# Performance work log

Measured on AMD Instinct MI355X. Metric: run time of the kernel, lower is better.

Reference implementation:

```python
import jax, jax.numpy as jnp
import numpy as np

N_NODES = 32768
N_EDGES = 524288
IN_F = 256
OUT_F = 128
NB = 4


def setup_inputs() -> dict:
    key = jax.random.key(0)
    ks = jax.random.split(key, 12)
    s_in = 1.0 / np.sqrt(IN_F)
    s_out = 1.0 / np.sqrt(OUT_F)
    s_cat = 1.0 / np.sqrt(OUT_F * NB)
    return {
        "x": jax.random.normal(ks[0], (N_NODES, IN_F), dtype=jnp.float32),
        "edge_index": jax.random.randint(ks[1], (2, N_EDGES), 0, N_NODES, dtype=jnp.int64),
        "Wb": jax.random.uniform(ks[2], (NB, IN_F, OUT_F), jnp.float32, -s_in, s_in),
        "bb": jax.random.uniform(ks[3], (NB, OUT_F), jnp.float32, -s_in, s_in),
        "W1": jax.random.uniform(ks[4], (NB, OUT_F, OUT_F), jnp.float32, -s_out, s_out),
        "b1": jax.random.uniform(ks[5], (NB, OUT_F), jnp.float32, -s_out, s_out),
        "W2": jax.random.uniform(ks[6], (NB, OUT_F, OUT_F), jnp.float32, -s_out, s_out),
        "b2": jax.random.uniform(ks[7], (NB, OUT_F), jnp.float32, -s_out, s_out),
        "branch_gates": jnp.ones((NB,), dtype=jnp.float32),
        "temperature": jnp.asarray(1.0, dtype=jnp.float32),
        "Wo": jax.random.uniform(ks[8], (OUT_F * NB, OUT_F), jnp.float32, -s_cat, s_cat),
        "bo": jax.random.uniform(ks[9], (OUT_F,), jnp.float32, -s_cat, s_cat),
    }


def _scatter_mean_step(h, row, col, inv_deg):
    # gather per-edge source features, mean-reduce onto destination nodes
    sums = jax.ops.segment_sum(h[row], col, num_segments=N_NODES)
    return sums * inv_deg


def reference(x, edge_index, Wb, bb, W1, b1, W2, b2, branch_gates, temperature, Wo, bo):
    row, col = edge_index[0], edge_index[1]
    deg = jax.ops.segment_sum(jnp.ones((N_EDGES,), x.dtype), col, num_segments=N_NODES)
    inv_deg = (1.0 / jnp.maximum(deg, 1.0))[:, None]  # empty segments -> 0 (scatter_mean semantics)

    gates = jax.nn.softmax(branch_gates / temperature)

    branch_outputs = []
    for i in range(NB):
        h = x @ Wb[i] + bb[i]                   # [N, OUT_F]
        for _ in range(i):                       # scale = scales[i % 4] = i
            h = _scatter_mean_step(h, row, col, inv_deg)
        h = jax.nn.relu(h @ W1[i] + b1[i]) @ W2[i] + b2[i]
        branch_outputs.append(h * gates[i])

    concat = jnp.concatenate(branch_outputs, axis=1)  # [N, NB*OUT_F]
    return concat @ Wo + bo
```

## Files before the change

### kernel.cpp

```cpp
#include <hip/hip_runtime.h>
#include <math.h>

#define N_NODES 32768
#define N_EDGES 524288
#define IN_F    256
#define OUT_F   128
#define NB      4

typedef __attribute__((ext_vector_type(8))) short bf16x8;
typedef __attribute__((ext_vector_type(4))) float f32x4;

__device__ __forceinline__ ushort f2b(float f) {
    uint u = __float_as_uint(f);
    return (ushort)((u + 0x7fffu + ((u >> 16) & 1u)) >> 16);
}
__device__ __forceinline__ float b2f_lo(uint v) { return __uint_as_float(v << 16); }
__device__ __forceinline__ float b2f_hi(uint v) { return __uint_as_float(v & 0xffff0000u); }

__device__ __forceinline__ float softmax_gate(const float* bg, const float* temp, int i) {
    float T = temp[0];
    float mx = fmaxf(fmaxf(bg[0], bg[1]), fmaxf(bg[2], bg[3]));
    float e0 = expf((bg[0] - mx) / T), e1 = expf((bg[1] - mx) / T);
    float e2 = expf((bg[2] - mx) / T), e3 = expf((bg[3] - mx) / T);
    float s = e0 + e1 + e2 + e3;
    float ei = (i == 0) ? e0 : (i == 1) ? e1 : (i == 2) ? e2 : e3;
    return ei / s;
}

__global__ void detect_kernel(const int* __restrict__ ei, int* __restrict__ flag) {
    int t = threadIdx.x;
    if (ei[2 * t + 1] != 0) atomicOr(flag, 1);
}

__global__ __launch_bounds__(256) void count_conv_kernel(
    const int* __restrict__ ei, const int* __restrict__ flag, int* __restrict__ deg,
    const float* __restrict__ x, ushort* __restrict__ xb) {
    int b = blockIdx.x;
    if (b < N_EDGES / 256) {
        int e = b * 256 + threadIdx.x;
        int c = (*flag == 0) ? ei[2 * (N_EDGES + e)] : ei[N_EDGES + e];
        atomicAdd(&deg[c], 1);
    } else {
        int idx = (b - N_EDGES / 256) * 256 + threadIdx.x;
        float4 v = ((const float4*)x)[idx];
        ushort4 o;
        o.x = f2b(v.x); o.y = f2b(v.y); o.z = f2b(v.z); o.w = f2b(v.w);
        ((ushort4*)xb)[idx] = o;
    }
}

__global__ __launch_bounds__(256) void scan1_kernel(const int* __restrict__ deg,
                                                    int* __restrict__ bsum) {
    int t = threadIdx.x;
    int v = deg[blockIdx.x * 256 + t];
    __shared__ int red[4];
    int lane = t & 63, wv = t >> 6;
#pragma unroll
    for (int off = 32; off > 0; off >>= 1) v += __shfl_down(v, off);
    if (lane == 0) red[wv] = v;
    __syncthreads();
    if (t == 0) bsum[blockIdx.x] = red[0] + red[1] + red[2] + red[3];
}

__global__ __launch_bounds__(128) void scan2_kernel(const int* __restrict__ bsum,
                                                    int* __restrict__ bbase,
                                                    int* __restrict__ offs) {
    __shared__ int s[128];
    int t = threadIdx.x;
    int v = bsum[t];
    s[t] = v;
    __syncthreads();
    for (int off = 1; off < 128; off <<= 1) {
        int add = (t >= off) ? s[t - off] : 0;
        __syncthreads();
        s[t] += add;
        __syncthreads();
    }
    bbase[t] = s[t] - v;
    if (t == 127) offs[N_NODES] = s[127];
}

__global__ __launch_bounds__(256) void scan3_kernel(
    const int* __restrict__ deg, const int* __restrict__ bbase,
    int* __restrict__ offs, int* __restrict__ cursor,
    float* __restrict__ invd, float* __restrict__ m1) {
    __shared__ int s[256];
    int t = threadIdx.x;
    int idx = blockIdx.x * 256 + t;
    int d = deg[idx];
    s[t] = d;
    __syncthreads();
    for (int off = 1; off < 256; off <<= 1) {
        int add = (t >= off) ? s[t - off] : 0;
        __syncthreads();
        s[t] += add;
        __syncthreads();
    }
    int excl = bbase[blockIdx.x] + s[t] - d;
    offs[idx] = excl;
    cursor[idx] = excl;
    invd[idx] = 1.0f / (float)((d > 1) ? d : 1);
    m1[idx] = (d > 0) ? 1.0f : 0.0f;
}

__global__ __launch_bounds__(256) void fill_prep_kernel(
    const int* __restrict__ ei, const int* __restrict__ flag,
    int* __restrict__ cursor, int* __restrict__ srcs,
    const float* __restrict__ Wb, const float* __restrict__ W1,
    const float* __restrict__ W2, const float* __restrict__ Wo,
    const float* __restrict__ bb, const float* __restrict__ b2,
    const float* __restrict__ bo, const float* __restrict__ bg,
    const float* __restrict__ temp,
    ushort* __restrict__ WcT, ushort* __restrict__ WzT,
    float* __restrict__ u, float* __restrict__ cvec) {
    __shared__ float smem[16 * 128];
    int b = blockIdx.x;
    int tid = threadIdx.x;
    if (b < N_EDGES / 256) {
        int e = b * 256 + tid;
        int r, c;
        if (*flag == 0) { r = ei[2 * e]; c = ei[2 * (N_EDGES + e)]; }
        else            { r = ei[e];     c = ei[N_EDGES + e]; }
        int slot = atomicAdd(&cursor[c], 1);
        srcs[slot] = r;
        return;
    }
    int f = tid & 127, rh = tid >> 7;
    if (b < N_EDGES / 256 + 64) {
        int id = b - N_EDGES / 256;
        int i = id >> 4, k0 = (id & 15) * 16;
#pragma unroll
        for (int rr = 0; rr < 8; rr++)
            smem[(rh * 8 + rr) * 128 + f] = Wb[((size_t)i * IN_F + k0 + rh * 8 + rr) * OUT_F + f];
        __syncthreads();
        float acc[8] = {};
        const float* W1i = W1 + (size_t)i * OUT_F * OUT_F;
        for (int j = 0; j < OUT_F; j++) {
            float w1 = W1i[j * OUT_F + f];
#pragma unroll
            for (int rr = 0; rr < 8; rr++) acc[rr] += smem[(rh * 8 + rr) * 128 + j] * w1;
        }
        ushort tmp[8];
#pragma unroll
        for (int rr = 0; rr < 8; rr++) tmp[rr] = f2b(acc[rr]);
        *(uint4*)(WcT + ((size_t)i * OUT_F + f) * IN_F + k0 + rh * 8) = *(uint4*)tmp;
    } else if (b < N_EDGES / 256 + 96) {
        int id = b - (N_EDGES / 256 + 64);
        int i = id >> 3, j0 = (id & 7) * 16;
#pragma unroll
        for (int rr = 0; rr < 8; rr++)
            smem[(rh * 8 + rr) * 128 + f] = W2[((size_t)i * OUT_F + j0 + rh * 8 + rr) * OUT_F + f];
        __syncthreads();
        float acc[8] = {};
        for (int l = 0; l < OUT_F; l++) {
            float wo = Wo[((size_t)i * OUT_F + l) * OUT_F + f];
#pragma unroll
            for (int rr = 0; rr < 8; rr++) acc[rr] += smem[(rh * 8 + rr) * 128 + l] * wo;
        }
        float g = softmax_gate(bg, temp, i);
        ushort tmp[8];
#pragma unroll
        for (int rr = 0; rr < 8; rr++) tmp[rr] = f2b(g * acc[rr]);
        *(uint4*)(WzT + (size_t)f * (NB * OUT_F) + i * OUT_F + j0 + rh * 8) = *(uint4*)tmp;
    } else {
        int id = b - (N_EDGES / 256 + 96);
        int jc = rh;
        if (id < NB) {
            int i = id;
            float partial = 0.f;
            for (int j = jc * 64; j < jc * 64 + 64; j++)
                partial += bb[i * OUT_F + j] * W1[((size_t)i * OUT_F + j) * OUT_F + f];
            smem[jc * 128 + f] = partial;
            __syncthreads();
            if (jc == 0) u[i * OUT_F + f] = smem[f] + smem[128 + f];
        } else {
            int i = id - NB;
            float partial = 0.f;
            for (int j = jc * 64; j < jc * 64 + 64; j++)
                partial += b2[i * OUT_F + j] * Wo[((size_t)i * OUT_F + j) * OUT_F + f];
            smem[jc * 128 + f] = partial;
            __syncthreads();
            if (jc == 0) {
                float tot = (smem[f] + smem[128 + f]) * softmax_gate(bg, temp, i);
                if (i == 0) tot += bo[f];
                atomicAdd(&cvec[f], tot);
            }
        }
    }
}

#define GATHER_256(INBUF)                                                       \
    float a0[8] = {0.f,0.f,0.f,0.f,0.f,0.f,0.f,0.f};                            \
    float a1[8] = {0.f,0.f,0.f,0.f,0.f,0.f,0.f,0.f};                            \
    int p = s;                                                                  \
    for (; p + 8 <= e; p += 8) {                                                \
        int base = p + 4 * half;                                                \
        int2 s01 = *(const int2*)(srcs + base);                                 \
        int2 s23 = *(const int2*)(srcs + base + 2);                             \
        uint4 v0 = *(const uint4*)(INBUF + (size_t)s01.x * IN_F + fl * 8);      \
        uint4 v1 = *(const uint4*)(INBUF + (size_t)s01.y * IN_F + fl * 8);      \
        uint4 v2 = *(const uint4*)(INBUF + (size_t)s23.x * IN_F + fl * 8);      \
        uint4 v3 = *(const uint4*)(INBUF + (size_t)s23.y * IN_F + fl * 8);      \
        ACC8(a0, v0); ACC8(a1, v1); ACC8(a0, v2); ACC8(a1, v3);                 \
    }                                                                           \
    for (; p + 4 <= e; p += 4) {                                                \
        int2 ss = *(const int2*)(srcs + p + 2 * half);                          \
        uint4 v0 = *(const uint4*)(INBUF + (size_t)ss.x * IN_F + fl * 8);       \
        uint4 v1 = *(const uint4*)(INBUF + (size_t)ss.y * IN_F + fl * 8);       \
        ACC8(a0, v0); ACC8(a1, v1);                                             \
    }                                                                           \
    for (; p + half < e; p += 2) {                                              \
        int src = srcs[p + half];                                               \
        uint4 v0 = *(const uint4*)(INBUF + (size_t)src * IN_F + fl * 8);        \
        ACC8(a0, v0);                                                           \
    }                                                                           \
    _Pragma("unroll") for (int k = 0; k < 8; k++) a0[k] += a1[k];               \
    _Pragma("unroll") for (int k = 0; k < 8; k++) a0[k] += __shfl_down(a0[k], 32);

#define ACC8(A, V)                                                              \
    A[0] += b2f_lo(V.x); A[1] += b2f_hi(V.x);                                   \
    A[2] += b2f_lo(V.y); A[3] += b2f_hi(V.y);                                   \
    A[4] += b2f_lo(V.z); A[5] += b2f_hi(V.z);                                   \
    A[6] += b2f_lo(V.w); A[7] += b2f_hi(V.w)

__global__ __launch_bounds__(256) void prop_x_kernel(
    const ushort* __restrict__ in, ushort* __restrict__ out,
    const float* __restrict__ m_in, float* __restrict__ m_out,
    const int* __restrict__ offs, const int* __restrict__ srcs,
    const float* __restrict__ invd) {
    int blk = blockIdx.x;
    if (blk >= N_NODES / 4) {
        int n = (blk - N_NODES / 4) * 256 + threadIdx.x;
        int s = offs[n], e = offs[n + 1];
        float sum = 0.f;
        for (int p = s; p < e; ++p) sum += m_in[srcs[p]];
        m_out[n] = sum * invd[n];
        return;
    }
    int node = blk * 4 + (threadIdx.x >> 6);
    int lane = threadIdx.x & 63;
    int half = lane >> 5, fl = lane & 31;
    int s = offs[node], e = offs[node + 1];
    GATHER_256(in);
    if (half == 0) {
        float w = invd[node];
        uint4 o;
        o.x = (uint)f2b(a0[0] * w) | ((uint)f2b(a0[1] * w) << 16);
        o.y = (uint)f2b(a0[2] * w) | ((uint)f2b(a0[3] * w) << 16);
        o.z = (uint)f2b(a0[4] * w) | ((uint)f2b(a0[5] * w) << 16);
        o.w = (uint)f2b(a0[6] * w) | ((uint)f2b(a0[7] * w) << 16);
        *(uint4*)(out + (size_t)node * IN_F + fl * 8) = o;
    }
}

__global__ __launch_bounds__(256) void prop_pq_kernel(
    const ushort* __restrict__ PQ, ushort* __restrict__ R, ushort* __restrict__ Qp,
    const float* __restrict__ m2, float* __restrict__ m3,
    const float* __restrict__ u2, const float* __restrict__ b12,
    const int* __restrict__ offs, const int* __restrict__ srcs,
    const float* __restrict__ invd) {
    int blk = blockIdx.x;
    if (blk >= N_NODES / 4) {
        int n = (blk - N_NODES / 4) * 256 + threadIdx.x;
        int s = offs[n], e = offs[n + 1];
        float sum = 0.f;
        for (int p = s; p < e; ++p) sum += m2[srcs[p]];
        m3[n] = sum * invd[n];
        return;
    }
    int node = blk * 4 + (threadIdx.x >> 6);
    int lane = threadIdx.x & 63;
    int half = lane >> 5, fl = lane & 31;
    int s = offs[node], e = offs[node + 1];
    GATHER_256(PQ);
    if (half == 0) {
        float w = invd[node];
        if (fl < 16) {
            int col = fl * 8;
            float mv = m2[node];
            float4 ua = *(const float4*)(u2 + col);
            float4 ub = *(const float4*)(u2 + col + 4);
            float4 ba = *(const float4*)(b12 + col);
            float4 bb_ = *(const float4*)(b12 + col + 4);
            float o_[8];
            o_[0] = fmaxf(a0[0] * w + mv * ua.x + ba.x, 0.f);
            o_[1] = fmaxf(a0[1] * w + mv * ua.y + ba.y, 0.f);
            o_[2] = fmaxf(a0[2] * w + mv * ua.z + ba.z, 0.f);
            o_[3] = fmaxf(a0[3] * w + mv * ua.w + ba.w, 0.f);
            o_[4] = fmaxf(a0[4] * w + mv * ub.x + bb_.x, 0.f);
            o_[5] = fmaxf(a0[5] * w + mv * ub.y + bb_.y, 0.f);
            o_[6] = fmaxf(a0[6] * w + mv * ub.z + bb_.z, 0.f);
            o_[7] = fmaxf(a0[7] * w + mv * ub.w + bb_.w, 0.f);
            uint4 o;
            o.x = (uint)f2b(o_[0]) | ((uint)f2b(o_[1]) << 16);
            o.y = (uint)f2b(o_[2]) | ((uint)f2b(o_[3]) << 16);
            o.z = (uint)f2b(o_[4]) | ((uint)f2b(o_[5]) << 16);
            o.w = (uint)f2b(o_[6]) | ((uint)f2b(o_[7]) << 16);
            *(uint4*)(R + (size_t)node * (NB * OUT_F) + 2 * OUT_F + col) = o;
        } else {
            int col = (fl - 16) * 8;
            uint4 o;
            o.x = (uint)f2b(a0[0] * w) | ((uint)f2b(a0[1] * w) << 16);
            o.y = (uint)f2b(a0[2] * w) | ((uint)f2b(a0[3] * w) << 16);
            o.z = (uint)f2b(a0[4] * w) | ((uint)f2b(a0[5] * w) << 16);
            o.w = (uint)f2b(a0[6] * w) | ((uint)f2b(a0[7] * w) << 16);
            *(uint4*)(Qp + (size_t)node * OUT_F + col) = o;
        }
    }
}

__global__ __launch_bounds__(256) void prop_q_kernel(
    const ushort* __restrict__ Qp, ushort* __restrict__ R,
    const float* __restrict__ m3, const float* __restrict__ u3,
    const float* __restrict__ b13,
    const int* __restrict__ offs, const int* __restrict__ srcs,
    const float* __restrict__ invd) {
    int node = blockIdx.x * 4 + (threadIdx.x >> 6);
    int lane = threadIdx.x & 63;
    int q = lane >> 4, fl = lane & 15;
    int s = offs[node], e = offs[node + 1];
    float a[8] = {0.f,0.f,0.f,0.f,0.f,0.f,0.f,0.f};
    float b[8] = {0.f,0.f,0.f,0.f,0.f,0.f,0.f,0.f};
    int p = s;
    for (; p + 8 <= e; p += 8) {
        int2 ss = *(const int2*)(srcs + p + 2 * q);
        uint4 v0 = *(const uint4*)(Qp + (size_t)ss.x * OUT_F + fl * 8);
        uint4 v1 = *(const uint4*)(Qp + (size_t)ss.y * OUT_F + fl * 8);
        ACC8(a, v0); ACC8(b, v1);
    }
    for (; p + 4 <= e; p += 4) {
        int src = srcs[p + q];
        uint4 v0 = *(const uint4*)(Qp + (size_t)src * OUT_F + fl * 8);
        ACC8(a, v0);
    }
    if (p + q < e) {
        int src = srcs[p + q];
        uint4 v0 = *(const uint4*)(Qp + (size_t)src * OUT_F + fl * 8);
        ACC8(a, v0);
    }
#pragma unroll
    for (int k = 0; k < 8; k++) a[k] += b[k];
#pragma unroll
    for (int k = 0; k < 8; k++) a[k] += __shfl_down(a[k], 32);
#pragma unroll
    for (int k = 0; k < 8; k++) a[k] += __shfl_down(a[k], 16);
    if (lane < 16) {
        float w = invd[node];
        float mv = m3[node];
        int col = fl * 8;
        float4 ua = *(const float4*)(u3 + col);
        float4 ub = *(const float4*)(u3 + col + 4);
        float4 ba = *(const float4*)(b13 + col);
        float4 bb_ = *(const float4*)(b13 + col + 4);
        float o_[8];
        o_[0] = fmaxf(a[0] * w + mv * ua.x + ba.x, 0.f);
        o_[1] = fmaxf(a[1] * w + mv * ua.y + ba.y, 0.f);
        o_[2] = fmaxf(a[2] * w + mv * ua.z + ba.z, 0.f);
        o_[3] = fmaxf(a[3] * w + mv * ua.w + ba.w, 0.f);
        o_[4] = fmaxf(a[4] * w + mv * ub.x + bb_.x, 0.f);
        o_[5] = fmaxf(a[5] * w + mv * ub.y + bb_.y, 0.f);
        o_[6] = fmaxf(a[6] * w + mv * ub.z + bb_.z, 0.f);
        o_[7] = fmaxf(a[7] * w + mv * ub.w + bb_.w, 0.f);
        uint4 o;
        o.x = (uint)f2b(o_[0]) | ((uint)f2b(o_[1]) << 16);
        o.y = (uint)f2b(o_[2]) | ((uint)f2b(o_[3]) << 16);
        o.z = (uint)f2b(o_[4]) | ((uint)f2b(o_[5]) << 16);
        o.w = (uint)f2b(o_[6]) | ((uint)f2b(o_[7]) << 16);
        *(uint4*)(R + (size_t)node * (NB * OUT_F) + 3 * OUT_F + col) = o;
    }
}

__global__ __launch_bounds__(256) void gemmP_kernel(
    const ushort* __restrict__ xb, const ushort* __restrict__ X1b,
    const ushort* __restrict__ WcT, const float* __restrict__ u,
    const float* __restrict__ b1, const float* __restrict__ m1,
    ushort* __restrict__ R, ushort* __restrict__ PQ) {
    int y = blockIdx.y;
    const ushort* A = (y == 0) ? xb : X1b;
    const ushort* WT = WcT + (size_t)y * OUT_F * IN_F;
    int m0 = blockIdx.x * 128;

    __shared__ ushort As[128][72];
    __shared__ ushort Bs[128][72];

    int tid = threadIdx.x;
    int wv = tid >> 6, lane = tid & 63, quad = lane >> 4, lm = lane & 15;

    f32x4 acc[2][8];
    f32x4 zero = {0.f, 0.f, 0.f, 0.f};
#pragma unroll
    for (int i = 0; i < 2; i++)
#pragma unroll
        for (int j = 0; j < 8; j++) acc[i][j] = zero;

    for (int k0 = 0; k0 < IN_F; k0 += 64) {
        __syncthreads();
#pragma unroll
        for (int it = 0; it < 4; it++) {
            int c = tid + 256 * it;
            int r = c >> 3, c8 = c & 7;
            *(uint4*)&As[r][c8 * 8] = *(const uint4*)(A + (size_t)(m0 + r) * IN_F + k0 + c8 * 8);
            *(uint4*)&Bs[r][c8 * 8] = *(const uint4*)(WT + (size_t)r * IN_F + k0 + c8 * 8);
        }
        __syncthreads();
#pragma unroll
        for (int ks = 0; ks < 2; ks++) {
            bf16x8 af0 = *(const bf16x8*)&As[wv * 32 + lm][ks * 32 + quad * 8];
            bf16x8 af1 = *(const bf16x8*)&As[wv * 32 + 16 + lm][ks * 32 + quad * 8];
#pragma unroll
            for (int nt = 0; nt < 8; nt++) {
                bf16x8 bf = *(const bf16x8*)&Bs[nt * 16 + lm][ks * 32 + quad * 8];
                acc[0][nt] = __builtin_amdgcn_mfma_f32_16x16x32_bf16(af0, bf, acc[0][nt], 0, 0, 0);
                acc[1][nt] = __builtin_amdgcn_mfma_f32_16x16x32_bf16(af1, bf, acc[1][nt], 0, 0, 0);
            }
        }
    }

    if (y >= 2) {
        int pqoff = (y - 2) * OUT_F;
#pragma unroll
        for (int mt = 0; mt < 2; mt++)
#pragma unroll
            for (int r = 0; r < 4; r++) {
                int row = m0 + wv * 32 + mt * 16 + quad * 4 + r;
#pragma unroll
                for (int nt = 0; nt < 8; nt++) {
                    int col = nt * 16 + lm;
                    PQ[(size_t)row * IN_F + pqoff + col] = f2b(acc[mt][nt][r]);
                }
            }
    } else {
        float uv[8], bv[8];
#pragma unroll
        for (int nt = 0; nt < 8; nt++) {
            int col = nt * 16 + lm;
            uv[nt] = u[y * OUT_F + col];
            bv[nt] = b1[y * OUT_F + col];
        }
#pragma unroll
        for (int mt = 0; mt < 2; mt++)
#pragma unroll
            for (int r = 0; r < 4; r++) {
                int row = m0 + wv * 32 + mt * 16 + quad * 4 + r;
                float mval = (y == 0) ? 1.0f : m1[row];
#pragma unroll
                for (int nt = 0; nt < 8; nt++) {
                    int col = nt * 16 + lm;
                    float h = acc[mt][nt][r] + mval * uv[nt] + bv[nt];
                    R[(size_t)row * (NB * OUT_F) + y * OUT_F + col] = f2b(fmaxf(h, 0.f));
                }
            }
    }
}

__global__ __launch_bounds__(256) void gemm2_mfma_kernel(
    const ushort* __restrict__ R, const ushort* __restrict__ WzT,
    const float* __restrict__ cvec, float* __restrict__ out) {
    int m0 = blockIdx.x * 128;
    const int K = NB * OUT_F;

    __shared__ ushort As[128][72];
    __shared__ ushort Bs[128][72];

    int tid = threadIdx.x;
    int wv = tid >> 6, lane = tid & 63, quad = lane >> 4, lm = lane & 15;

    f32x4 acc[2][8];
    f32x4 zero = {0.f, 0.f, 0.f, 0.f};
#pragma unroll
    for (int i = 0; i < 2; i++)
#pragma unroll
        for (int j = 0; j < 8; j++) acc[i][j] = zero;

    for (int k0 = 0; k0 < K; k0 += 64) {
        __syncthreads();
#pragma unroll
        for (int it = 0; it < 4; it++) {
            int c = tid + 256 * it;
            int r = c >> 3, c8 = c & 7;
            *(uint4*)&As[r][c8 * 8] = *(const uint4*)(R + (size_t)(m0 + r) * K + k0 + c8 * 8);
            *(uint4*)&Bs[r][c8 * 8] = *(const uint4*)(WzT + (size_t)r * K + k0 + c8 * 8);
        }
        __syncthreads();
#pragma unroll
        for (int ks = 0; ks < 2; ks++) {
            bf16x8 af0 = *(const bf16x8*)&As[wv * 32 + lm][ks * 32 + quad * 8];
            bf16x8 af1 = *(const bf16x8*)&As[wv * 32 + 16 + lm][ks * 32 + quad * 8];
#pragma unroll
            for (int nt = 0; nt < 8; nt++) {
                bf16x8 bf = *(const bf16x8*)&Bs[nt * 16 + lm][ks * 32 + quad * 8];
                acc[0][nt] = __builtin_amdgcn_mfma_f32_16x16x32_bf16(af0, bf, acc[0][nt], 0, 0, 0);
                acc[1][nt] = __builtin_amdgcn_mfma_f32_16x16x32_bf16(af1, bf, acc[1][nt], 0, 0, 0);
            }
        }
    }

    float cb[8];
#pragma unroll
    for (int nt = 0; nt < 8; nt++) cb[nt] = cvec[nt * 16 + lm];
#pragma unroll
    for (int mt = 0; mt < 2; mt++)
#pragma unroll
        for (int r = 0; r < 4; r++) {
            int row = m0 + wv * 32 + mt * 16 + quad * 4 + r;
#pragma unroll
            for (int nt = 0; nt < 8; nt++) {
                int col = nt * 16 + lm;
                out[(size_t)row * OUT_F + col] = acc[mt][nt][r] + cb[nt];
            }
        }
}

extern "C" void kernel_launch(void* const* d_in, const int* in_sizes, int n_in,
                              void* d_out, int out_size, void* d_ws, size_t ws_size,
                              hipStream_t stream) {
    const float* x    = (const float*)d_in[0];
    const int*   ei   = (const int*)d_in[1];
    const float* Wb   = (const float*)d_in[2];
    const float* bb   = (const float*)d_in[3];
    const float* W1   = (const float*)d_in[4];
    const float* b1   = (const float*)d_in[5];
    const float* W2   = (const float*)d_in[6];
    const float* b2   = (const float*)d_in[7];
    const float* bg   = (const float*)d_in[8];
    const float* temp = (const float*)d_in[9];
    const float* Wo   = (const float*)d_in[10];
    const float* bo   = (const float*)d_in[11];
    float* out = (float*)d_out;

    char* w = (char*)d_ws;
    size_t used = 0;
    auto alloc = [&](size_t bytes) {
        char* p = w + used;
        used += (bytes + 255) & ~(size_t)255;
        return p;
    };
    int*    deg    = (int*)alloc(N_NODES * 4);
    float*  cvec   = (float*)alloc(OUT_F * 4);
    int*    flag   = (int*)alloc(4);
    int*    offs   = (int*)alloc((N_NODES + 2) * 4);
    int*    cursor = (int*)alloc(N_NODES * 4);
    int*    srcs   = (int*)alloc(N_EDGES * 4);
    int*    bsum   = (int*)alloc(128 * 4);
    int*    bbase  = (int*)alloc(128 * 4);
    float*  invd   = (float*)alloc(N_NODES * 4);
    float*  mbuf   = (float*)alloc((size_t)3 * N_NODES * 4);
    float*  u      = (float*)alloc(NB * OUT_F * 4);
    ushort* WcT    = (ushort*)alloc((size_t)NB * IN_F * OUT_F * 2);
    ushort* WzT    = (ushort*)alloc((size_t)NB * OUT_F * OUT_F * 2);
    ushort* xb     = (ushort*)alloc((size_t)N_NODES * IN_F * 2);
    ushort* X1b    = (ushort*)alloc((size_t)N_NODES * IN_F * 2);
    ushort* PQ     = (ushort*)alloc((size_t)N_NODES * IN_F * 2);
    ushort* Qp     = (ushort*)alloc((size_t)N_NODES * OUT_F * 2);
    ushort* R      = (ushort*)alloc((size_t)N_NODES * NB * OUT_F * 2);
    if (used > ws_size) return;

    float* m1v = mbuf;
    float* m2v = mbuf + N_NODES;
    float* m3v = mbuf + 2 * N_NODES;

    hipMemsetAsync(deg, 0, N_NODES * 4 + 512 + 256, stream);

    detect_kernel<<<1, 64, 0, stream>>>(ei, flag);
    count_conv_kernel<<<N_EDGES / 256 + N_NODES * IN_F / 1024, 256, 0, stream>>>(
        ei, flag, deg, x, xb);
    scan1_kernel<<<N_NODES / 256, 256, 0, stream>>>(deg, bsum);
    scan2_kernel<<<1, 128, 0, stream>>>(bsum, bbase, offs);
    scan3_kernel<<<N_NODES / 256, 256, 0, stream>>>(deg, bbase, offs, cursor, invd, m1v);
    fill_prep_kernel<<<N_EDGES / 256 + 64 + 32 + 8, 256, 0, stream>>>(
        ei, flag, cursor, srcs, Wb, W1, W2, Wo, bb, b2, bo, bg, temp, WcT, WzT, u, cvec);

    prop_x_kernel<<<N_NODES / 4 + N_NODES / 256, 256, 0, stream>>>(
        xb, X1b, m1v, m2v, offs, srcs, invd);
    {
        dim3 grid(N_NODES / 128, NB);
        gemmP_kernel<<<grid, 256, 0, stream>>>(xb, X1b, WcT, u, b1, m1v, R, PQ);
    }
    prop_pq_kernel<<<N_NODES / 4 + N_NODES / 256, 256, 0, stream>>>(
        PQ, R, Qp, m2v, m3v, u + 2 * OUT_F, b1 + 2 * OUT_F, offs, srcs, invd);
    prop_q_kernel<<<N_NODES / 4, 256, 0, stream>>>(
        Qp, R, m3v, u + 3 * OUT_F, b1 + 3 * OUT_F, offs, srcs, invd);

    gemm2_mfma_kernel<<<N_NODES / 128, 256, 0, stream>>>(R, WzT, cvec, out);
}
```

Baseline: 308.4 us.

## Fuse independent GEMM tiles into gather kernels and merge prep launches

Moves branch-0 and branch-1 GEMMs into the gather/propagation kernels as extra blocks so the compute-bound MFMA tiles can run alongside memory-bound gathers. Only the branch-2/3 GEMM stays as a separate launch. The int32/int64 detection is folded into each kernel via a ballot, removing the detect launch and flag buffer. Weight prep and bf16 conversion now share a launch with degree counting, and the CSR fill becomes its own kernel. The cost is larger, more heterogeneous grids, higher LDS and register use per block for the gather blocks, and block-scheduling imbalance.

```diff
diff --git a/kernel.cpp b/kernel.cpp
--- a/kernel.cpp
+++ b/kernel.cpp
@@ -6,6 +6,12 @@
 #define IN_F    256
 #define OUT_F   128
 #define NB      4
+
+#define NE_BLK   (N_EDGES / 256)
+#define CONV_BLK (N_NODES * IN_F / 1024)
+#define GX_BLK   (N_NODES / 4)
+#define GEMM_BLK (N_NODES / 128)
+#define M_BLK    (N_NODES / 256)
 
 typedef __attribute__((ext_vector_type(8))) short bf16x8;
 typedef __attribute__((ext_vector_type(4))) float f32x4;
@@ -27,85 +33,18 @@
     return ei / s;
 }
 
-__global__ void detect_kernel(const int* __restrict__ ei, int* __restrict__ flag) {
-    int t = threadIdx.x;
-    if (ei[2 * t + 1] != 0) atomicOr(flag, 1);
-}
-
-__global__ __launch_bounds__(256) void count_conv_kernel(
-    const int* __restrict__ ei, const int* __restrict__ flag, int* __restrict__ deg,
-    const float* __restrict__ x, ushort* __restrict__ xb) {
-    int b = blockIdx.x;
-    if (b < N_EDGES / 256) {
-        int e = b * 256 + threadIdx.x;
-        int c = (*flag == 0) ? ei[2 * (N_EDGES + e)] : ei[N_EDGES + e];
-        atomicAdd(&deg[c], 1);
-    } else {
-        int idx = (b - N_EDGES / 256) * 256 + threadIdx.x;
-        float4 v = ((const float4*)x)[idx];
-        ushort4 o;
-        o.x = f2b(v.x); o.y = f2b(v.y); o.z = f2b(v.z); o.w = f2b(v.w);
-        ((ushort4*)xb)[idx] = o;
-    }
-}
-
-__global__ __launch_bounds__(256) void scan1_kernel(const int* __restrict__ deg,
-                                                    int* __restrict__ bsum) {
-    int t = threadIdx.x;
-    int v = deg[blockIdx.x * 256 + t];
-    __shared__ int red[4];
-    int lane = t & 63, wv = t >> 6;
-#pragma unroll
-    for (int off = 32; off > 0; off >>= 1) v += __shfl_down(v, off);
-    if (lane == 0) red[wv] = v;
+__device__ __forceinline__ int detect_i32(const int* __restrict__ ei, int* sflag) {
+    if (threadIdx.x < 64) {
+        unsigned long long b = __ballot(ei[2 * threadIdx.x + 1] != 0);
+        if (threadIdx.x == 0) *sflag = (b != 0ull) ? 1 : 0;
+    }
     __syncthreads();
-    if (t == 0) bsum[blockIdx.x] = red[0] + red[1] + red[2] + red[3];
-}
-
-__global__ __launch_bounds__(128) void scan2_kernel(const int* __restrict__ bsum,
-                                                    int* __restrict__ bbase,
-                                                    int* __restrict__ offs) {
-    __shared__ int s[128];
-    int t = threadIdx.x;
-    int v = bsum[t];
-    s[t] = v;
-    __syncthreads();
-    for (int off = 1; off < 128; off <<= 1) {
-        int add = (t >= off) ? s[t - off] : 0;
-        __syncthreads();
-        s[t] += add;
-        __syncthreads();
-    }
-    bbase[t] = s[t] - v;
-    if (t == 127) offs[N_NODES] = s[127];
-}
-
-__global__ __launch_bounds__(256) void scan3_kernel(
-    const int* __restrict__ deg, const int* __restrict__ bbase,
-    int* __restrict__ offs, int* __restrict__ cursor,
-    float* __restrict__ invd, float* __restrict__ m1) {
-    __shared__ int s[256];
-    int t = threadIdx.x;
-    int idx = blockIdx.x * 256 + t;
-    int d = deg[idx];
-    s[t] = d;
-    __syncthreads();
-    for (int off = 1; off < 256; off <<= 1) {
-        int add = (t >= off) ? s[t - off] : 0;
-        __syncthreads();
-        s[t] += add;
-        __syncthreads();
-    }
-    int excl = bbase[blockIdx.x] + s[t] - d;
-    offs[idx] = excl;
-    cursor[idx] = excl;
-    invd[idx] = 1.0f / (float)((d > 1) ? d : 1);
-    m1[idx] = (d > 0) ? 1.0f : 0.0f;
-}
-
-__global__ __launch_bounds__(256) void fill_prep_kernel(
-    const int* __restrict__ ei, const int* __restrict__ flag,
-    int* __restrict__ cursor, int* __restrict__ srcs,
+    return *sflag;
+}
+
+__global__ __launch_bounds__(256) void count_prep_kernel(
+    const int* __restrict__ ei, int* __restrict__ deg,
+    const float* __restrict__ x, ushort* __restrict__ xb,
     const float* __restrict__ Wb, const float* __restrict__ W1,
     const float* __restrict__ W2, const float* __restrict__ Wo,
     const float* __restrict__ bb, const float* __restrict__ b2,
@@ -114,21 +53,29 @@
     ushort* __restrict__ WcT, ushort* __restrict__ WzT,
     float* __restrict__ u, float* __restrict__ cvec) {
     __shared__ float smem[16 * 128];
+    __shared__ int sflag;
     int b = blockIdx.x;
     int tid = threadIdx.x;
-    if (b < N_EDGES / 256) {
+    if (b < NE_BLK) {
+        int i32 = detect_i32(ei, &sflag);
         int e = b * 256 + tid;
-        int r, c;
-        if (*flag == 0) { r = ei[2 * e]; c = ei[2 * (N_EDGES + e)]; }
-        else            { r = ei[e];     c = ei[N_EDGES + e]; }
-        int slot = atomicAdd(&cursor[c], 1);
-        srcs[slot] = r;
+        int c = (i32 == 0) ? ei[2 * (N_EDGES + e)] : ei[N_EDGES + e];
+        atomicAdd(&deg[c], 1);
         return;
     }
+    b -= NE_BLK;
+    if (b < CONV_BLK) {
+        int idx = b * 256 + tid;
+        float4 v = ((const float4*)x)[idx];
+        ushort4 o;
+        o.x = f2b(v.x); o.y = f2b(v.y); o.z = f2b(v.z); o.w = f2b(v.w);
+        ((ushort4*)xb)[idx] = o;
+        return;
+    }
+    b -= CONV_BLK;
     int f = tid & 127, rh = tid >> 7;
-    if (b < N_EDGES / 256 + 64) {
-        int id = b - N_EDGES / 256;
-        int i = id >> 4, k0 = (id & 15) * 16;
+    if (b < 64) {
+        int i = b >> 4, k0 = (b & 15) * 16;
 #pragma unroll
         for (int rr = 0; rr < 8; rr++)
             smem[(rh * 8 + rr) * 128 + f] = Wb[((size_t)i * IN_F + k0 + rh * 8 + rr) * OUT_F + f];
@@ -144,8 +91,8 @@
 #pragma unroll
         for (int rr = 0; rr < 8; rr++) tmp[rr] = f2b(acc[rr]);
         *(uint4*)(WcT + ((size_t)i * OUT_F + f) * IN_F + k0 + rh * 8) = *(uint4*)tmp;
-    } else if (b < N_EDGES / 256 + 96) {
-        int id = b - (N_EDGES / 256 + 64);
+    } else if (b < 96) {
+        int id = b - 64;
         int i = id >> 3, j0 = (id & 7) * 16;
 #pragma unroll
         for (int rr = 0; rr < 8; rr++)
@@ -163,7 +110,7 @@
         for (int rr = 0; rr < 8; rr++) tmp[rr] = f2b(g * acc[rr]);
         *(uint4*)(WzT + (size_t)f * (NB * OUT_F) + i * OUT_F + j0 + rh * 8) = *(uint4*)tmp;
     } else {
-        int id = b - (N_EDGES / 256 + 96);
+        int id = b - 96;
         int jc = rh;
         if (id < NB) {
             int i = id;
@@ -188,6 +135,78 @@
         }
     }
 }
+
+__global__ __launch_bounds__(256) void scan1_kernel(const int* __restrict__ deg,
+                                                    int* __restrict__ bsum) {
+    int t = threadIdx.x;
+    int v = deg[blockIdx.x * 256 + t];
+    __shared__ int red[4];
+    int lane = t & 63, wv = t >> 6;
+#pragma unroll
+    for (int off = 32; off > 0; off >>= 1) v += __shfl_down(v, off);
+    if (lane == 0) red[wv] = v;
+    __syncthreads();
+    if (t == 0) bsum[blockIdx.x] = red[0] + red[1] + red[2] + red[3];
+}
+
+__global__ __launch_bounds__(128) void scan2_kernel(const int* __restrict__ bsum,
+                                                    int* __restrict__ bbase,
+                                                    int* __restrict__ offs) {
+    __shared__ int s[128];
+    int t = threadIdx.x;
+    int v = bsum[t];
+    s[t] = v;
+    __syncthreads();
+    for (int off = 1; off < 128; off <<= 1) {
+        int add = (t >= off) ? s[t - off] : 0;
+        __syncthreads();
+        s[t] += add;
+        __syncthreads();
+    }
+    bbase[t] = s[t] - v;
+    if (t == 127) offs[N_NODES] = s[127];
+}
+
+__global__ __launch_bounds__(256) void scan3_kernel(
+    const int* __restrict__ deg, const int* __restrict__ bbase,
+    int* __restrict__ offs, int* __restrict__ cursor,
+    float* __restrict__ invd, float* __restrict__ m1) {
+    __shared__ int s[256];
+    int t = threadIdx.x;
+    int idx = blockIdx.x * 256 + t;
+    int d = deg[idx];
+    s[t] = d;
+    __syncthreads();
+    for (int off = 1; off < 256; off <<= 1) {
+        int add = (t >= off) ? s[t - off] : 0;
+        __syncthreads();
+        s[t] += add;
+        __syncthreads();
+    }
+    int excl = bbase[blockIdx.x] + s[t] - d;
+    offs[idx] = excl;
+    cursor[idx] = excl;
+    invd[idx] = 1.0f / (float)((d > 1) ? d : 1);
+    m1[idx] = (d > 0) ? 1.0f : 0.0f;
+}
+
+__global__ __launch_bounds__(256) void fill_kernel(
+    const int* __restrict__ ei, int* __restrict__ cursor, int* __restrict__ srcs) {
+    __shared__ int sflag;
+    int i32 = detect_i32(ei, &sflag);
+    int e = blockIdx.x * 256 + threadIdx.x;
+    int r, c;
+    if (i32 == 0) { r = ei[2 * e]; c = ei[2 * (N_EDGES + e)]; }
+    else          { r = ei[e];     c = ei[N_EDGES + e]; }
+    int slot = atomicAdd(&cursor[c], 1);
+    srcs[slot] = r;
+}
+
+#define ACC8(A, V)                                                              \
+    A[0] += b2f_lo(V.x); A[1] += b2f_hi(V.x);                                   \
+    A[2] += b2f_lo(V.y); A[3] += b2f_hi(V.y);                                   \
+    A[4] += b2f_lo(V.z); A[5] += b2f_hi(V.z);                                   \
+    A[6] += b2f_lo(V.w); A[7] += b2f_hi(V.w)
 
 #define GATHER_256(INBUF)                                                       \
     float a0[8] = {0.f,0.f,0.f,0.f,0.f,0.f,0.f,0.f};                            \
@@ -217,31 +236,81 @@
     _Pragma("unroll") for (int k = 0; k < 8; k++) a0[k] += a1[k];               \
     _Pragma("unroll") for (int k = 0; k < 8; k++) a0[k] += __shfl_down(a0[k], 32);
 
-#define ACC8(A, V)                                                              \
-    A[0] += b2f_lo(V.x); A[1] += b2f_hi(V.x);                                   \
-    A[2] += b2f_lo(V.y); A[3] += b2f_hi(V.y);                                   \
-    A[4] += b2f_lo(V.z); A[5] += b2f_hi(V.z);                                   \
-    A[6] += b2f_lo(V.w); A[7] += b2f_hi(V.w)
-
-__global__ __launch_bounds__(256) void prop_x_kernel(
-    const ushort* __restrict__ in, ushort* __restrict__ out,
-    const float* __restrict__ m_in, float* __restrict__ m_out,
+#define GEMM_TILE_BODY(APTR, WTPTR, UPTR, BPTR, MEXPR, RCOL)                    \
+    int m0 = gblk * 128;                                                        \
+    int wv = tid >> 6, lane = tid & 63, quad = lane >> 4, lm = lane & 15;       \
+    f32x4 acc[2][8];                                                            \
+    f32x4 zero = {0.f, 0.f, 0.f, 0.f};                                          \
+    _Pragma("unroll") for (int i = 0; i < 2; i++)                               \
+        _Pragma("unroll") for (int j = 0; j < 8; j++) acc[i][j] = zero;         \
+    for (int k0 = 0; k0 < IN_F; k0 += 64) {                                     \
+        __syncthreads();                                                        \
+        _Pragma("unroll") for (int it = 0; it < 4; it++) {                      \
+            int c = tid + 256 * it;                                             \
+            int r = c >> 3, c8 = c & 7;                                         \
+            *(uint4*)&As[r][c8 * 8] =                                           \
+                *(const uint4*)(APTR + (size_t)(m0 + r) * IN_F + k0 + c8 * 8);  \
+            *(uint4*)&Bs[r][c8 * 8] =                                           \
+                *(const uint4*)(WTPTR + (size_t)r * IN_F + k0 + c8 * 8);        \
+        }                                                                       \
+        __syncthreads();                                                        \
+        _Pragma("unroll") for (int ks = 0; ks < 2; ks++) {                      \
+            bf16x8 af0 = *(const bf16x8*)&As[wv * 32 + lm][ks * 32 + quad * 8]; \
+            bf16x8 af1 = *(const bf16x8*)&As[wv * 32 + 16 + lm][ks * 32 + quad * 8]; \
+            _Pragma("unroll") for (int nt = 0; nt < 8; nt++) {                  \
+                bf16x8 bf = *(const bf16x8*)&Bs[nt * 16 + lm][ks * 32 + quad * 8]; \
+                acc[0][nt] = __builtin_amdgcn_mfma_f32_16x16x32_bf16(af0, bf, acc[0][nt], 0, 0, 0); \
+                acc[1][nt] = __builtin_amdgcn_mfma_f32_16x16x32_bf16(af1, bf, acc[1][nt], 0, 0, 0); \
+            }                                                                   \
+        }                                                                       \
+    }                                                                           \
+    float uv[8], bv[8];                                                         \
+    _Pragma("unroll") for (int nt = 0; nt < 8; nt++) {                          \
+        int col = nt * 16 + lm;                                                 \
+        uv[nt] = UPTR[col];                                                     \
+        bv[nt] = BPTR[col];                                                     \
+    }                                                                           \
+    _Pragma("unroll") for (int mt = 0; mt < 2; mt++)                            \
+        _Pragma("unroll") for (int r = 0; r < 4; r++) {                         \
+            int row = m0 + wv * 32 + mt * 16 + quad * 4 + r;                    \
+            float mval = (MEXPR);                                               \
+            _Pragma("unroll") for (int nt = 0; nt < 8; nt++) {                  \
+                int col = nt * 16 + lm;                                         \
+                float h = acc[mt][nt][r] + mval * uv[nt] + bv[nt];              \
+                R[(size_t)row * (NB * OUT_F) + (RCOL) + col] = f2b(fmaxf(h, 0.f)); \
+            }                                                                   \
+        }
+
+__global__ __launch_bounds__(256) void prop_x_gemm0_kernel(
+    const ushort* __restrict__ xb, ushort* __restrict__ X1b,
+    const float* __restrict__ m1, float* __restrict__ m2,
+    const ushort* __restrict__ WcT, const float* __restrict__ u,
+    const float* __restrict__ b1, ushort* __restrict__ R,
     const int* __restrict__ offs, const int* __restrict__ srcs,
     const float* __restrict__ invd) {
+    __shared__ ushort As[128][72];
+    __shared__ ushort Bs[128][72];
     int blk = blockIdx.x;
-    if (blk >= N_NODES / 4) {
-        int n = (blk - N_NODES / 4) * 256 + threadIdx.x;
+    int tid = threadIdx.x;
+    if (blk < GEMM_BLK) {
+        int gblk = blk;
+        GEMM_TILE_BODY(xb, WcT, u, b1, 1.0f, 0)
+        return;
+    }
+    blk -= GEMM_BLK;
+    if (blk >= GX_BLK) {
+        int n = (blk - GX_BLK) * 256 + tid;
         int s = offs[n], e = offs[n + 1];
         float sum = 0.f;
-        for (int p = s; p < e; ++p) sum += m_in[srcs[p]];
-        m_out[n] = sum * invd[n];
+        for (int p = s; p < e; ++p) sum += m1[srcs[p]];
+        m2[n] = sum * invd[n];
         return;
     }
-    int node = blk * 4 + (threadIdx.x >> 6);
-    int lane = threadIdx.x & 63;
+    int node = blk * 4 + (tid >> 6);
+    int lane = tid & 63;
     int half = lane >> 5, fl = lane & 31;
     int s = offs[node], e = offs[node + 1];
-    GATHER_256(in);
+    GATHER_256(xb);
     if (half == 0) {
         float w = invd[node];
         uint4 o;
@@ -249,27 +318,94 @@
         o.y = (uint)f2b(a0[2] * w) | ((uint)f2b(a0[3] * w) << 16);
         o.z = (uint)f2b(a0[4] * w) | ((uint)f2b(a0[5] * w) << 16);
         o.w = (uint)f2b(a0[6] * w) | ((uint)f2b(a0[7] * w) << 16);
-        *(uint4*)(out + (size_t)node * IN_F + fl * 8) = o;
-    }
-}
-
-__global__ __launch_bounds__(256) void prop_pq_kernel(
-    const ushort* __restrict__ PQ, ushort* __restrict__ R, ushort* __restrict__ Qp,
-    const float* __restrict__ m2, float* __restrict__ m3,
-    const float* __restrict__ u2, const float* __restrict__ b12,
+        *(uint4*)(X1b + (size_t)node * IN_F + fl * 8) = o;
+    }
+}
+
+__global__ __launch_bounds__(256) void gemmP23_kernel(
+    const ushort* __restrict__ X1b, const ushort* __restrict__ WcT,
+    ushort* __restrict__ PQ) {
+    int y = blockIdx.y + 2;
+    const ushort* WT = WcT + (size_t)y * OUT_F * IN_F;
+    int m0 = blockIdx.x * 128;
+    __shared__ ushort As[128][72];
+    __shared__ ushort Bs[128][72];
+    int tid = threadIdx.x;
+    int wv = tid >> 6, lane = tid & 63, quad = lane >> 4, lm = lane & 15;
+    f32x4 acc[2][8];
+    f32x4 zero = {0.f, 0.f, 0.f, 0.f};
+#pragma unroll
+    for (int i = 0; i < 2; i++)
+#pragma unroll
+        for (int j = 0; j < 8; j++) acc[i][j] = zero;
+    for (int k0 = 0; k0 < IN_F; k0 += 64) {
+        __syncthreads();
+#pragma unroll
+        for (int it = 0; it < 4; it++) {
+            int c = tid + 256 * it;
+            int r = c >> 3, c8 = c & 7;
+            *(uint4*)&As[r][c8 * 8] = *(const uint4*)(X1b + (size_t)(m0 + r) * IN_F + k0 + c8 * 8);
+            *(uint4*)&Bs[r][c8 * 8] = *(const uint4*)(WT + (size_t)r * IN_F + k0 + c8 * 8);
+        }
+        __syncthreads();
+#pragma unroll
+        for (int ks = 0; ks < 2; ks++) {
+            bf16x8 af0 = *(const bf16x8*)&As[wv * 32 + lm][ks * 32 + quad * 8];
+            bf16x8 af1 = *(const bf16x8*)&As[wv * 32 + 16 + lm][ks * 32 + quad * 8];
+#pragma unroll
+            for (int nt = 0; nt < 8; nt++) {
+                bf16x8 bf = *(const bf16x8*)&Bs[nt * 16 + lm][ks * 32 + quad * 8];
+                acc[0][nt] = __builtin_amdgcn_mfma_f32_16x16x32_bf16(af0, bf, acc[0][nt], 0, 0, 0);
+                acc[1][nt] = __builtin_amdgcn_mfma_f32_16x16x32_bf16(af1, bf, acc[1][nt], 0, 0, 0);
+            }
+        }
+    }
+    int pqoff = (y - 2) * OUT_F;
+#pragma unroll
+    for (int mt = 0; mt < 2; mt++)
+#pragma unroll
+        for (int r = 0; r < 4; r++) {
+            int row = m0 + wv * 32 + mt * 16 + quad * 4 + r;
+#pragma unroll
+            for (int nt = 0; nt < 8; nt++) {
+                int col = nt * 16 + lm;
+                PQ[(size_t)row * IN_F + pqoff + col] = f2b(acc[mt][nt][r]);
+            }
+        }
+}
+
+__global__ __launch_bounds__(256) void prop_pq_gemm1_kernel(
+    const ushort* __restrict__ PQ, const ushort* __restrict__ X1b,
+    ushort* __restrict__ R, ushort* __restrict__ Qp,
+    const float* __restrict__ m1, const float* __restrict__ m2,
+    float* __restrict__ m3,
+    const ushort* __restrict__ WcT, const float* __restrict__ u,
+    const float* __restrict__ b1,
     const int* __restrict__ offs, const int* __restrict__ srcs,
     const float* __restrict__ invd) {
+    __shared__ ushort As[128][72];
+    __shared__ ushort Bs[128][72];
     int blk = blockIdx.x;
-    if (blk >= N_NODES / 4) {
-        int n = (blk - N_NODES / 4) * 256 + threadIdx.x;
+    int tid = threadIdx.x;
+    if (blk < GEMM_BLK) {
+        int gblk = blk;
+        const ushort* WT1 = WcT + (size_t)1 * OUT_F * IN_F;
+        const float* u1 = u + OUT_F;
+        const float* b11 = b1 + OUT_F;
+        GEMM_TILE_BODY(X1b, WT1, u1, b11, m1[row], OUT_F)
+        return;
+    }
+    blk -= GEMM_BLK;
+    if (blk >= GX_BLK) {
+        int n = (blk - GX_BLK) * 256 + tid;
         int s = offs[n], e = offs[n + 1];
         float sum = 0.f;
         for (int p = s; p < e; ++p) sum += m2[srcs[p]];
         m3[n] = sum * invd[n];
         return;
     }
-    int node = blk * 4 + (threadIdx.x >> 6);
-    int lane = threadIdx.x & 63;
+    int node = blk * 4 + (tid >> 6);
+    int lane = tid & 63;
     int half = lane >> 5, fl = lane & 31;
     int s = offs[node], e = offs[node + 1];
     GATHER_256(PQ);
@@ -278,6 +414,8 @@
         if (fl < 16) {
             int col = fl * 8;
             float mv = m2[node];
+            const float* u2 = u + 2 * OUT_F;
+            const float* b12 = b1 + 2 * OUT_F;
             float4 ua = *(const float4*)(u2 + col);
             float4 ub = *(const float4*)(u2 + col + 4);
             float4 ba = *(const float4*)(b12 + col);
@@ -370,37 +508,29 @@
     }
 }
 
-__global__ __launch_bounds__(256) void gemmP_kernel(
-    const ushort* __restrict__ xb, const ushort* __restrict__ X1b,
-    const ushort* __restrict__ WcT, const float* __restrict__ u,
-    const float* __restrict__ b1, const float* __restrict__ m1,
-    ushort* __restrict__ R, ushort* __restrict__ PQ) {
-    int y = blockIdx.y;
-    const ushort* A = (y == 0) ? xb : X1b;
-    const ushort* WT = WcT + (size_t)y * OUT_F * IN_F;
+__global__ __launch_bounds__(256) void gemm2_mfma_kernel(
+    const ushort* __restrict__ R, const ushort* __restrict__ WzT,
+    const float* __restrict__ cvec, float* __restrict__ out) {
     int m0 = blockIdx.x * 128;
-
+    const int K = NB * OUT_F;
     __shared__ ushort As[128][72];
     __shared__ ushort Bs[128][72];
-
     int tid = threadIdx.x;
     int wv = tid >> 6, lane = tid & 63, quad = lane >> 4, lm = lane & 15;
-
     f32x4 acc[2][8];
     f32x4 zero = {0.f, 0.f, 0.f, 0.f};
 #pragma unroll
     for (int i = 0; i < 2; i++)
 #pragma unroll
         for (int j = 0; j < 8; j++) acc[i][j] = zero;
-
-    for (int k0 = 0; k0 < IN_F; k0 += 64) {
+    for (int k0 = 0; k0 < K; k0 += 64) {
         __syncthreads();
 #pragma unroll
         for (int it = 0; it < 4; it++) {
             int c = tid + 256 * it;
             int r = c >> 3, c8 = c & 7;
-            *(uint4*)&As[r][c8 * 8] = *(const uint4*)(A + (size_t)(m0 + r) * IN_F + k0 + c8 * 8);
-            *(uint4*)&Bs[r][c8 * 8] = *(const uint4*)(WT + (size_t)r * IN_F + k0 + c8 * 8);
+            *(uint4*)&As[r][c8 * 8] = *(const uint4*)(R + (size_t)(m0 + r) * K + k0 + c8 * 8);
+            *(uint4*)&Bs[r][c8 * 8] = *(const uint4*)(WzT + (size_t)r * K + k0 + c8 * 8);
         }
         __syncthreads();
 #pragma unroll
@@ -415,86 +545,6 @@
             }
         }
     }
-
-    if (y >= 2) {
-        int pqoff = (y - 2) * OUT_F;
-#pragma unroll
-        for (int mt = 0; mt < 2; mt++)
-#pragma unroll
-            for (int r = 0; r < 4; r++) {
-                int row = m0 + wv * 32 + mt * 16 + quad * 4 + r;
-#pragma unroll
-                for (int nt = 0; nt < 8; nt++) {
-                    int col = nt * 16 + lm;
-                    PQ[(size_t)row * IN_F + pqoff + col] = f2b(acc[mt][nt][r]);
-                }
-            }
-    } else {
-        float uv[8], bv[8];
-#pragma unroll
-        for (int nt = 0; nt < 8; nt++) {
-            int col = nt * 16 + lm;
-            uv[nt] = u[y * OUT_F + col];
-            bv[nt] = b1[y * OUT_F + col];
-        }
-#pragma unroll
-        for (int mt = 0; mt < 2; mt++)
-#pragma unroll
-            for (int r = 0; r < 4; r++) {
-                int row = m0 + wv * 32 + mt * 16 + quad * 4 + r;
-                float mval = (y == 0) ? 1.0f : m1[row];
-#pragma unroll
-                for (int nt = 0; nt < 8; nt++) {
-                    int col = nt * 16 + lm;
-                    float h = acc[mt][nt][r] + mval * uv[nt] + bv[nt];
-                    R[(size_t)row * (NB * OUT_F) + y * OUT_F + col] = f2b(fmaxf(h, 0.f));
-                }
-            }
-    }
-}
-
-__global__ __launch_bounds__(256) void gemm2_mfma_kernel(
-    const ushort* __restrict__ R, const ushort* __restrict__ WzT,
-    const float* __restrict__ cvec, float* __restrict__ out) {
-    int m0 = blockIdx.x * 128;
-    const int K = NB * OUT_F;
-
-    __shared__ ushort As[128][72];
-    __shared__ ushort Bs[128][72];
-
-    int tid = threadIdx.x;
-    int wv = tid >> 6, lane = tid & 63, quad = lane >> 4, lm = lane & 15;
-
-    f32x4 acc[2][8];
-    f32x4 zero = {0.f, 0.f, 0.f, 0.f};
-#pragma unroll
-    for (int i = 0; i < 2; i++)
-#pragma unroll
-        for (int j = 0; j < 8; j++) acc[i][j] = zero;
-
-    for (int k0 = 0; k0 < K; k0 += 64) {
-        __syncthreads();
-#pragma unroll
-        for (int it = 0; it < 4; it++) {
-            int c = tid + 256 * it;
-            int r = c >> 3, c8 = c & 7;
-            *(uint4*)&As[r][c8 * 8] = *(const uint4*)(R + (size_t)(m0 + r) * K + k0 + c8 * 8);
-            *(uint4*)&Bs[r][c8 * 8] = *(const uint4*)(WzT + (size_t)r * K + k0 + c8 * 8);
-        }
-        __syncthreads();
-#pragma unroll
-        for (int ks = 0; ks < 2; ks++) {
-            bf16x8 af0 = *(const bf16x8*)&As[wv * 32 + lm][ks * 32 + quad * 8];
-            bf16x8 af1 = *(const bf16x8*)&As[wv * 32 + 16 + lm][ks * 32 + quad * 8];
-#pragma unroll
-            for (int nt = 0; nt < 8; nt++) {
-                bf16x8 bf = *(const bf16x8*)&Bs[nt * 16 + lm][ks * 32 + quad * 8];
-                acc[0][nt] = __builtin_amdgcn_mfma_f32_16x16x32_bf16(af0, bf, acc[0][nt], 0, 0, 0);
-                acc[1][nt] = __builtin_amdgcn_mfma_f32_16x16x32_bf16(af1, bf, acc[1][nt], 0, 0, 0);
-            }
-        }
-    }
-
     float cb[8];
 #pragma unroll
     for (int nt = 0; nt < 8; nt++) cb[nt] = cvec[nt * 16 + lm];
@@ -537,7 +587,6 @@
     };
     int*    deg    = (int*)alloc(N_NODES * 4);
     float*  cvec   = (float*)alloc(OUT_F * 4);
-    int*    flag   = (int*)alloc(4);
     int*    offs   = (int*)alloc((N_NODES + 2) * 4);
     int*    cursor = (int*)alloc(N_NODES * 4);
     int*    srcs   = (int*)alloc(N_EDGES * 4);
@@ -559,25 +608,23 @@
     float* m2v = mbuf + N_NODES;
     float* m3v = mbuf + 2 * N_NODES;
 
-    hipMemsetAsync(deg, 0, N_NODES * 4 + 512 + 256, stream);
-
-    detect_kernel<<<1, 64, 0, stream>>>(ei, flag);
-    count_conv_kernel<<<N_EDGES / 256 + N_NODES * IN_F / 1024, 256, 0, stream>>>(
-        ei, flag, deg, x, xb);
+    hipMemsetAsync(deg, 0, N_NODES * 4 + 512, stream);
+
+    count_prep_kernel<<<NE_BLK + CONV_BLK + 104, 256, 0, stream>>>(
+        ei, deg, x, xb, Wb, W1, W2, Wo, bb, b2, bo, bg, temp, WcT, WzT, u, cvec);
     scan1_kernel<<<N_NODES / 256, 256, 0, stream>>>(deg, bsum);
     scan2_kernel<<<1, 128, 0, stream>>>(bsum, bbase, offs);
     scan3_kernel<<<N_NODES / 256, 256, 0, stream>>>(deg, bbase, offs, cursor, invd, m1v);
-    fill_prep_kernel<<<N_EDGES / 256 + 64 + 32 + 8, 256, 0, stream>>>(
-        ei, flag, cursor, srcs, Wb, W1, W2, Wo, bb, b2, bo, bg, temp, WcT, WzT, u, cvec);
-
-    prop_x_kernel<<<N_NODES / 4 + N_NODES / 256, 256, 0, stream>>>(
-        xb, X1b, m1v, m2v, offs, srcs, invd);
+    fill_kernel<<<NE_BLK, 256, 0, stream>>>(ei, cursor, srcs);
+
+    prop_x_gemm0_kernel<<<GEMM_BLK + GX_BLK + M_BLK, 256, 0, stream>>>(
+        xb, X1b, m1v, m2v, WcT, u, b1, R, offs, srcs, invd);
     {
-        dim3 grid(N_NODES / 128, NB);
-        gemmP_kernel<<<grid, 256, 0, stream>>>(xb, X1b, WcT, u, b1, m1v, R, PQ);
-    }
-    prop_pq_kernel<<<N_NODES / 4 + N_NODES / 256, 256, 0, stream>>>(
-        PQ, R, Qp, m2v, m3v, u + 2 * OUT_F, b1 + 2 * OUT_F, offs, srcs, invd);
+        dim3 grid(GEMM_BLK, 2);
+        gemmP23_kernel<<<grid, 256, 0, stream>>>(X1b, WcT, PQ);
+    }
+    prop_pq_gemm1_kernel<<<GEMM_BLK + GX_BLK + M_BLK, 256, 0, stream>>>(
+        PQ, X1b, R, Qp, m1v, m2v, m3v, WcT, u, b1, offs, srcs, invd);
     prop_q_kernel<<<N_NODES / 4, 256, 0, stream>>>(
         Qp, R, m3v, u + 3 * OUT_F, b1 + 3 * OUT_F, offs, srcs, invd);
 
```

New measurement: 340.1 us. 10.3% more time.
